# Optimization experiments

Measured on AMD Instinct MI355X. Metric: run time of the kernel, lower is better.

Reference implementation:

```python
import jax, jax.numpy as jnp
import numpy as np

B, IN, H, OUT = 1024, 512, 1024, 512   # tokens, input, hidden (MoE width), output
E, K, LAYERS = 8, 2, 10                 # experts, top-k, repeated MoE applications
EPS = 1e-10
LOSS_COEF = 0.01


def setup_inputs() -> dict:
    key = jax.random.key(0)
    ks = jax.random.split(key, 8)
    s = 0.02  # small init scale for weights
    return {
        "x": jax.random.normal(ks[0], (B, IN), jnp.float32),
        "enc_w": jax.random.normal(ks[1], (IN, H), jnp.float32) * s,
        "enc_b": jnp.zeros((H,), jnp.float32),
        "w_gate": jax.random.normal(ks[2], (H, E), jnp.float32) * s,
        "w1": jax.random.normal(ks[3], (E, H, H), jnp.float32) * s,
        "b1": jnp.zeros((E, H), jnp.float32),
        "w2": jax.random.normal(ks[4], (E, H, H), jnp.float32) * s,
        "b2": jnp.zeros((E, H), jnp.float32),
        "dec_w": jax.random.normal(ks[5], (H, OUT), jnp.float32) * s,
        "dec_b": jnp.zeros((OUT,), jnp.float32),
    }


def _cv_squared(v):
    # torch .var() is unbiased (ddof=1)
    return jnp.var(v, ddof=1) / (jnp.mean(v) ** 2 + EPS)


def _moe_layer(h, w_gate, w1, b1, w2, b2):
    # top-k gating (eval / no-noise path of noisy_top_k_gating)
    logits = h @ w_gate                                  # [B, E]
    top_vals, top_idx = jax.lax.top_k(logits, K)         # [B, K]
    gk = jax.nn.softmax(top_vals, axis=-1)               # softmax over top-k logits
    b = h.shape[0]
    gates = jnp.zeros((b, E), h.dtype).at[jnp.arange(b)[:, None], top_idx].set(gk)
    importance = gates.sum(axis=0)                       # [E]
    load = (gates > 0).sum(axis=0).astype(h.dtype)       # [E]
    aux = LOSS_COEF * (_cv_squared(importance) + _cv_squared(load))
    # experts: Linear -> ReLU -> Linear; combine weighted by gates
    # (dense-over-experts form; math identical to sparse dispatch/combine)
    hid = jax.nn.relu(jnp.einsum('bh,ehf->bef', h, w1) + b1)  # [B, E, H]
    y = jnp.einsum('bef,efo->beo', hid, w2) + b2              # [B, E, H]
    out = jnp.einsum('be,beo->bo', gates, y)                  # [B, H]
    return out, aux


def reference(x, enc_w, enc_b, w_gate, w1, b1, w2, b2, dec_w, dec_b):
    h = jax.nn.relu(x @ enc_w + enc_b)
    loss = jnp.zeros((), h.dtype)
    for _ in range(LAYERS):  # same MoE module (shared params) applied 10 times
        h, aux = _moe_layer(h, w_gate, w1, b1, w2, b2)
        loss = loss + aux
    out = jax.nn.relu(h @ dec_w + dec_b)
    return out, loss
```

## Files before the change

kernel.cpp:

```cpp
#include <hip/hip_runtime.h>
#include <math.h>

#define TPB 256
typedef unsigned short u16;
typedef unsigned int u32;
typedef __bf16 bf16x8 __attribute__((ext_vector_type(8)));
typedef float f32x4 __attribute__((ext_vector_type(4)));

namespace {
constexpr int NTOK  = 1024;
constexpr int IND   = 512;
constexpr int HD    = 1024;
constexpr int OUTD  = 512;
constexpr int NE    = 8;
constexpr int NSLOT = 2048;
}

__device__ __forceinline__ u16 f2bf(float f) {
  u32 x = __float_as_uint(f);
  x += 0x7fffu + ((x >> 16) & 1u);
  return (u16)(x >> 16);
}
__device__ __forceinline__ float bf2f(u16 u) { return __uint_as_float(((u32)u) << 16); }
__device__ __forceinline__ void split2(float v, u16& h, u16& l) {
  h = f2bf(v);
  l = f2bf(v - bf2f(h));
}

__device__ __forceinline__ void gll16(const void* g, void* l) {
  __builtin_amdgcn_global_load_lds((const __attribute__((address_space(1))) void*)g,
                                   (__attribute__((address_space(3))) void*)l, 16, 0, 0);
}


__global__ __launch_bounds__(TPB)
void transpose_split(const float* __restrict__ in, u16* __restrict__ ohi,
                     u16* __restrict__ olo, int K, int N)
{
  const int z = blockIdx.z;
  in  += (size_t)z * K * N;
  ohi += (size_t)z * K * N;
  olo += (size_t)z * K * N;
  __shared__ float tile[32][33];
  const int k0 = blockIdx.y * 32, n0 = blockIdx.x * 32;
  const int tx = threadIdx.x & 31, ty = threadIdx.x >> 5;
#pragma unroll
  for (int i = 0; i < 4; ++i) {
    int k = ty + i * 8;
    tile[k][tx] = in[(size_t)(k0 + k) * N + n0 + tx];
  }
  __syncthreads();
#pragma unroll
  for (int i = 0; i < 4; ++i) {
    int n = ty + i * 8;
    float v = tile[tx][n];
    u16 h, l; split2(v, h, l);
    int kk = k0 + tx, nn = n0 + n;
    size_t o = ((size_t)((nn >> 6) * (K >> 6) + (kk >> 6)) << 12)
             + (((nn & 63) * 8 + (((kk >> 3) & 7) ^ (nn & 7))) << 3) + (kk & 7);
    ohi[o] = h; olo[o] = l;
  }
}

__global__ __launch_bounds__(TPB)
void split_rows(const float* __restrict__ in, u16* __restrict__ oh,
                u16* __restrict__ ol, int nelem)
{
  int i = blockIdx.x * TPB + threadIdx.x;
  if (i * 4 >= nelem) return;
  float4 v = ((const float4*)in)[i];
  ushort4 H, L;
  split2(v.x, H.x, L.x); split2(v.y, H.y, L.y);
  split2(v.z, H.z, L.z); split2(v.w, H.w, L.w);
  ((ushort4*)oh)[i] = H;
  ((ushort4*)ol)[i] = L;
}

template<bool RELU, bool GROUPED, bool GATHER, bool SPLIT_OUT>
__global__ __launch_bounds__(TPB)
void gemm_split(const u16* __restrict__ Ah, const u16* __restrict__ Al,
                const int* __restrict__ gatherIdx,
                const u16* __restrict__ Bh, const u16* __restrict__ Bl,
                const float* __restrict__ bias,
                float* __restrict__ Cf, u16* __restrict__ Ch, u16* __restrict__ Cl,
                const int* __restrict__ seg_off, const int* __restrict__ seg_cnt,
                int M, int K, int N)
{
  const int e = GROUPED ? blockIdx.z : 0;
  int cnt = M, base = 0;
  if (GROUPED) { cnt = seg_cnt[e]; base = seg_off[e]; }
  const int tm = blockIdx.y, tn = blockIdx.x;
  if (tm * 64 >= cnt) return;

  __shared__ u16 smem[16384];
  constexpr int AHo = 0, ALo = 4096, BHo = 8192, BLo = 12288;

  const int t = threadIdx.x;
  const int wid = t >> 6, lane = t & 63;
  const int wr = wid >> 1, wc = wid & 1;

  const u16* aph[2]; const u16* apl[2];
#pragma unroll
  for (int i = 0; i < 2; ++i) {
    int slot = t + i * TPB;
    int row = slot >> 3, kblk = slot & 7;
    int kbs = kblk ^ (row & 7);
    int row_in = tm * 64 + row;
    int rv = row_in < cnt ? row_in : 0;
    int src;
    if (GATHER)      src = gatherIdx[base + rv];
    else             src = GROUPED ? base + rv : rv;
    size_t off = (size_t)src * K + kbs * 8;
    aph[i] = Ah + off; apl[i] = Al + off;
  }
  const u16* bsh; const u16* bsl;
  {
    size_t pb = ((size_t)((GROUPED ? e : 0) * (N >> 6) + tn) * (K >> 6)) << 12;
    bsh = Bh + pb; bsl = Bl + pb;
  }

  auto stage = [&](int ks) {
#pragma unroll
    for (int i = 0; i < 2; ++i) {
      int so = (t + i * TPB) * 8;
      gll16(aph[i] + (ks << 6), &smem[AHo + so]);
      gll16(apl[i] + (ks << 6), &smem[ALo + so]);
    }
    const size_t tb = (size_t)ks << 12;
#pragma unroll
    for (int i = 0; i < 2; ++i) {
      int so = (t + i * TPB) * 8;
      gll16(bsh + tb + so, &smem[BHo + so]);
      gll16(bsl + tb + so, &smem[BLo + so]);
    }
  };

  f32x4 acc[2][2];
#pragma unroll
  for (int i = 0; i < 2; ++i)
#pragma unroll
    for (int j = 0; j < 2; ++j) acc[i][j] = (f32x4){0.f, 0.f, 0.f, 0.f};

  auto compute = [&]() {
#pragma unroll
    for (int s = 0; s < 2; ++s) {
      const int kb = s * 4 + (lane >> 4);
      bf16x8 fah[2], fal[2];
#pragma unroll
      for (int fr = 0; fr < 2; ++fr) {
        int ar = wr * 32 + fr * 16 + (lane & 15);
        int off = ar * 64 + ((kb ^ (ar & 7)) << 3);
        fah[fr] = *(const bf16x8*)&smem[AHo + off];
        fal[fr] = *(const bf16x8*)&smem[ALo + off];
      }
      bf16x8 fbh[2], fbl[2];
#pragma unroll
      for (int fc = 0; fc < 2; ++fc) {
        int bn = wc * 32 + fc * 16 + (lane & 15);
        int off = bn * 64 + ((kb ^ (bn & 7)) << 3);
        fbh[fc] = *(const bf16x8*)&smem[BHo + off];
        fbl[fc] = *(const bf16x8*)&smem[BLo + off];
      }
      __builtin_amdgcn_s_setprio(1);
#pragma unroll
      for (int fr = 0; fr < 2; ++fr)
#pragma unroll
        for (int fc = 0; fc < 2; ++fc) {
          acc[fr][fc] = __builtin_amdgcn_mfma_f32_16x16x32_bf16(fah[fr], fbh[fc], acc[fr][fc], 0, 0, 0);
          acc[fr][fc] = __builtin_amdgcn_mfma_f32_16x16x32_bf16(fah[fr], fbl[fc], acc[fr][fc], 0, 0, 0);
          acc[fr][fc] = __builtin_amdgcn_mfma_f32_16x16x32_bf16(fal[fr], fbh[fc], acc[fr][fc], 0, 0, 0);
        }
      __builtin_amdgcn_s_setprio(0);
    }
  };

  const int NT = K >> 6;
  for (int ks = 0; ks < NT; ++ks) {
    stage(ks);
    __syncthreads();
    compute();
    __syncthreads();
  }

  const float* bp = bias + (GROUPED ? (size_t)e * N : 0);
#pragma unroll
  for (int fr = 0; fr < 2; ++fr) {
#pragma unroll
    for (int q = 0; q < 4; ++q) {
      int row_in = tm * 64 + wr * 32 + fr * 16 + ((lane >> 4) << 2) + q;
      if (row_in >= cnt) continue;
      size_t orow = (size_t)(GROUPED ? base + row_in : row_in);
#pragma unroll
      for (int fc = 0; fc < 2; ++fc) {
        int col = tn * 64 + wc * 32 + fc * 16 + (lane & 15);
        float v = acc[fr][fc][q] + bp[col];
        if (RELU) v = fmaxf(v, 0.f);
        if (SPLIT_OUT) {
          u16 h, l; split2(v, h, l);
          Ch[orow * N + col] = h;
          Cl[orow * N + col] = l;
        } else {
          Cf[orow * N + col] = v;
        }
      }
    }
  }
}

__global__ __launch_bounds__(TPB)
void gate_split(const u16* __restrict__ hh, const u16* __restrict__ hl,
                const float* __restrict__ w_gate,
                int* __restrict__ eidx, float* __restrict__ gval)
{
  const int b = blockIdx.x, t = threadIdx.x;
  ushort4 H = ((const ushort4*)(hh + (size_t)b * HD))[t];
  ushort4 L = ((const ushort4*)(hl + (size_t)b * HD))[t];
  float hv[4] = { bf2f(H.x) + bf2f(L.x), bf2f(H.y) + bf2f(L.y),
                  bf2f(H.z) + bf2f(L.z), bf2f(H.w) + bf2f(L.w) };
  float acc[NE] = {};
  const int i0 = t * 4;
#pragma unroll
  for (int j = 0; j < 4; ++j) {
    const float4* wg = (const float4*)(w_gate + (size_t)(i0 + j) * NE);
    float4 w0 = wg[0], w1 = wg[1];
    acc[0] = fmaf(hv[j], w0.x, acc[0]); acc[1] = fmaf(hv[j], w0.y, acc[1]);
    acc[2] = fmaf(hv[j], w0.z, acc[2]); acc[3] = fmaf(hv[j], w0.w, acc[3]);
    acc[4] = fmaf(hv[j], w1.x, acc[4]); acc[5] = fmaf(hv[j], w1.y, acc[5]);
    acc[6] = fmaf(hv[j], w1.z, acc[6]); acc[7] = fmaf(hv[j], w1.w, acc[7]);
  }
  __shared__ float red[TPB][NE];
#pragma unroll
  for (int e = 0; e < NE; ++e) red[t][e] = acc[e];
  __syncthreads();
  for (int s = TPB / 2; s > 0; s >>= 1) {
    if (t < s) {
#pragma unroll
      for (int e = 0; e < NE; ++e) red[t][e] += red[t + s][e];
    }
    __syncthreads();
  }
  if (t == 0) {
    float v1 = -1e30f; int e1 = 0;
#pragma unroll
    for (int e = 0; e < NE; ++e) { float v = red[0][e]; if (v > v1) { v1 = v; e1 = e; } }
    float v2 = -1e30f; int e2 = 0;
#pragma unroll
    for (int e = 0; e < NE; ++e) {
      if (e == e1) continue;
      float v = red[0][e]; if (v > v2) { v2 = v; e2 = e; }
    }
    float ev = expf(v2 - v1);
    eidx[b * 2] = e1;  eidx[b * 2 + 1] = e2;
    gval[b * 2] = 1.f / (1.f + ev);  gval[b * 2 + 1] = ev / (1.f + ev);
  }
}

__global__ __launch_bounds__(TPB)
void stats_scatter(const int* __restrict__ eidx, const float* __restrict__ gval,
                   float* __restrict__ loss, int* __restrict__ seg_off,
                   int* __restrict__ seg_cnt, int* __restrict__ slot_token,
                   int* __restrict__ slot_of)
{
  const int t = threadIdx.x;
  float imp[NE] = {};
  int   cnt[NE] = {};
  for (int s = t; s < NSLOT; s += TPB) {
    int e = eidx[s]; float g = gval[s];
#pragma unroll
    for (int q = 0; q < NE; ++q) if (q == e) { imp[q] += g; cnt[q]++; }
  }
  __shared__ float rimp[TPB][NE];
  __shared__ int   rcnt[TPB][NE];
#pragma unroll
  for (int e = 0; e < NE; ++e) { rimp[t][e] = imp[e]; rcnt[t][e] = cnt[e]; }
  __syncthreads();
  for (int s = TPB / 2; s > 0; s >>= 1) {
    if (t < s) {
#pragma unroll
      for (int e = 0; e < NE; ++e) { rimp[t][e] += rimp[t + s][e]; rcnt[t][e] += rcnt[t + s][e]; }
    }
    __syncthreads();
  }
  __shared__ int s_off[NE], s_fill[NE];
  if (t == 0) {
    float mi = 0.f, ml = 0.f;
#pragma unroll
    for (int e = 0; e < NE; ++e) { mi += rimp[0][e]; ml += (float)rcnt[0][e]; }
    mi /= NE; ml /= NE;
    float vi = 0.f, vl = 0.f;
#pragma unroll
    for (int e = 0; e < NE; ++e) {
      float di = rimp[0][e] - mi; vi += di * di;
      float dl = (float)rcnt[0][e] - ml; vl += dl * dl;
    }
    vi /= (NE - 1); vl /= (NE - 1);
    loss[0] += 0.01f * (vi / (mi * mi + 1e-10f) + vl / (ml * ml + 1e-10f));
    int off = 0;
#pragma unroll
    for (int e = 0; e < NE; ++e) {
      seg_off[e] = off; seg_cnt[e] = rcnt[0][e];
      s_off[e] = off; s_fill[e] = 0; off += rcnt[0][e];
    }
  }
  __syncthreads();
  for (int s = t; s < NSLOT; s += TPB) {
    int e = eidx[s];
    int pos = s_off[e] + atomicAdd(&s_fill[e], 1);
    slot_token[pos] = s >> 1;
    slot_of[s] = pos;
  }
}

template<bool GATE>
__global__ __launch_bounds__(TPB)
void combine_gate(const float* __restrict__ y, const float* __restrict__ gv_in,
                  const int* __restrict__ slot_of, const float* __restrict__ w_gate,
                  u16* __restrict__ hh, u16* __restrict__ hl,
                  int* __restrict__ eidx, float* __restrict__ gval)
{
  const int b = blockIdx.x, t = threadIdx.x;
  const int p0 = slot_of[b * 2], p1 = slot_of[b * 2 + 1];
  const float g0 = gv_in[b * 2], g1 = gv_in[b * 2 + 1];
  float4 a = ((const float4*)(y + (size_t)p0 * HD))[t];
  float4 c = ((const float4*)(y + (size_t)p1 * HD))[t];
  float v[4] = { g0 * a.x + g1 * c.x, g0 * a.y + g1 * c.y,
                 g0 * a.z + g1 * c.z, g0 * a.w + g1 * c.w };
  ushort4 H, L;
  split2(v[0], H.x, L.x); split2(v[1], H.y, L.y);
  split2(v[2], H.z, L.z); split2(v[3], H.w, L.w);
  ((ushort4*)(hh + (size_t)b * HD))[t] = H;
  ((ushort4*)(hl + (size_t)b * HD))[t] = L;

  if (GATE) {
    float acc[NE] = {};
    const int i0 = t * 4;
#pragma unroll
    for (int j = 0; j < 4; ++j) {
      const float4* wg = (const float4*)(w_gate + (size_t)(i0 + j) * NE);
      float4 w0 = wg[0], w1 = wg[1];
      acc[0] = fmaf(v[j], w0.x, acc[0]); acc[1] = fmaf(v[j], w0.y, acc[1]);
      acc[2] = fmaf(v[j], w0.z, acc[2]); acc[3] = fmaf(v[j], w0.w, acc[3]);
      acc[4] = fmaf(v[j], w1.x, acc[4]); acc[5] = fmaf(v[j], w1.y, acc[5]);
      acc[6] = fmaf(v[j], w1.z, acc[6]); acc[7] = fmaf(v[j], w1.w, acc[7]);
    }
    __shared__ float red[TPB][NE];
#pragma unroll
    for (int e = 0; e < NE; ++e) red[t][e] = acc[e];
    __syncthreads();
    for (int s = TPB / 2; s > 0; s >>= 1) {
      if (t < s) {
#pragma unroll
        for (int e = 0; e < NE; ++e) red[t][e] += red[t + s][e];
      }
      __syncthreads();
    }
    if (t == 0) {
      float v1 = -1e30f; int e1 = 0;
#pragma unroll
      for (int e = 0; e < NE; ++e) { float vv = red[0][e]; if (vv > v1) { v1 = vv; e1 = e; } }
      float v2 = -1e30f; int e2 = 0;
#pragma unroll
      for (int e = 0; e < NE; ++e) {
        if (e == e1) continue;
        float vv = red[0][e]; if (vv > v2) { v2 = vv; e2 = e; }
      }
      float ev = expf(v2 - v1);
      eidx[b * 2] = e1;  eidx[b * 2 + 1] = e2;
      gval[b * 2] = 1.f / (1.f + ev);  gval[b * 2 + 1] = ev / (1.f + ev);
    }
  }
}

__global__ void init_kernel(float* loss) { loss[0] = 0.f; }
__global__ void write_loss(const float* __restrict__ loss, float* __restrict__ out)
{ out[0] = loss[0]; }

template<bool RELU, bool GROUPED, bool GATHER>
__global__ __launch_bounds__(TPB)
void gemm_f32(const float* __restrict__ A, const int* __restrict__ gatherIdx,
              const float* __restrict__ B, const float* __restrict__ bias,
              float* __restrict__ C, const int* __restrict__ seg_off,
              const int* __restrict__ seg_cnt, int M, int K, int N)
{
  const int e = GROUPED ? blockIdx.z : 0;
  int cnt = M, base = 0;
  if (GROUPED) { cnt = seg_cnt[e]; base = seg_off[e]; }
  const int tm = blockIdx.y, tn = blockIdx.x;
  if (tm * 64 >= cnt) return;
  const float* Bp = B + (size_t)e * K * N;
  const float* bp = bias + (size_t)e * N;
  __shared__ float As[16][68];
  __shared__ float Bs[16][64];
  const int t = threadIdx.x;
  const int rm0 = (t >> 4) << 2, cn0 = (t & 15) << 2;
  int arow[4]; bool aval[4];
#pragma unroll
  for (int i = 0; i < 4; ++i) {
    int idx = t + i * TPB;
    int r = idx >> 4;
    int row_in = tm * 64 + r;
    bool v = row_in < cnt;
    int src;
    if (GATHER) src = v ? gatherIdx[base + row_in] : 0;
    else        src = v ? (GROUPED ? base + row_in : row_in) : 0;
    arow[i] = src; aval[i] = v;
  }
  float acc[4][4] = {};
  for (int k0 = 0; k0 < K; k0 += 16) {
#pragma unroll
    for (int i = 0; i < 4; ++i) {
      int idx = t + i * TPB;
      int r = idx >> 4, kk = idx & 15;
      As[kk][r] = aval[i] ? A[(size_t)arow[i] * K + k0 + kk] : 0.f;
    }
#pragma unroll
    for (int i = 0; i < 4; ++i) {
      int idx = t + i * TPB;
      int kk = idx >> 6, n = idx & 63;
      Bs[kk][n] = Bp[(size_t)(k0 + kk) * N + tn * 64 + n];
    }
    __syncthreads();
#pragma unroll
    for (int kk = 0; kk < 16; ++kk) {
      const float4 a4 = *(const float4*)&As[kk][rm0];
      const float4 b4 = *(const float4*)&Bs[kk][cn0];
      float av[4] = {a4.x, a4.y, a4.z, a4.w};
      float bv[4] = {b4.x, b4.y, b4.z, b4.w};
#pragma unroll
      for (int i = 0; i < 4; ++i)
#pragma unroll
        for (int j = 0; j < 4; ++j) acc[i][j] = fmaf(av[i], bv[j], acc[i][j]);
    }
    __syncthreads();
  }
#pragma unroll
  for (int i = 0; i < 4; ++i) {
    int row_in = tm * 64 + rm0 + i;
    if (row_in >= cnt) continue;
    size_t orow = (size_t)(base + row_in);
    float v0 = acc[i][0] + bp[tn * 64 + cn0 + 0];
    float v1 = acc[i][1] + bp[tn * 64 + cn0 + 1];
    float v2 = acc[i][2] + bp[tn * 64 + cn0 + 2];
    float v3 = acc[i][3] + bp[tn * 64 + cn0 + 3];
    if (RELU) { v0 = fmaxf(v0, 0.f); v1 = fmaxf(v1, 0.f); v2 = fmaxf(v2, 0.f); v3 = fmaxf(v3, 0.f); }
    *(float4*)&C[orow * N + tn * 64 + cn0] = make_float4(v0, v1, v2, v3);
  }
}

__global__ __launch_bounds__(TPB)
void gate_f32(const float* __restrict__ h, const float* __restrict__ w_gate,
              int* __restrict__ eidx, float* __restrict__ gval)
{
  const int b = blockIdx.x, t = threadIdx.x;
  float acc[NE] = {};
  const float* hb = h + (size_t)b * HD;
  for (int i = t; i < HD; i += TPB) {
    float hv = hb[i];
    const float* wg = w_gate + (size_t)i * NE;
#pragma unroll
    for (int e = 0; e < NE; ++e) acc[e] = fmaf(hv, wg[e], acc[e]);
  }
  __shared__ float red[TPB][NE];
#pragma unroll
  for (int e = 0; e < NE; ++e) red[t][e] = acc[e];
  __syncthreads();
  for (int s = TPB / 2; s > 0; s >>= 1) {
    if (t < s) {
#pragma unroll
      for (int e = 0; e < NE; ++e) red[t][e] += red[t + s][e];
    }
    __syncthreads();
  }
  if (t == 0) {
    float v1 = -1e30f; int e1 = 0;
#pragma unroll
    for (int e = 0; e < NE; ++e) { float v = red[0][e]; if (v > v1) { v1 = v; e1 = e; } }
    float v2 = -1e30f; int e2 = 0;
#pragma unroll
    for (int e = 0; e < NE; ++e) {
      if (e == e1) continue;
      float v = red[0][e]; if (v > v2) { v2 = v; e2 = e; }
    }
    float ev = expf(v2 - v1);
    eidx[b * 2] = e1;  eidx[b * 2 + 1] = e2;
    gval[b * 2] = 1.f / (1.f + ev);  gval[b * 2 + 1] = ev / (1.f + ev);
  }
}

__global__ __launch_bounds__(TPB)
void combine_f32(const float* __restrict__ y, const float* __restrict__ gval,
                 const int* __restrict__ slot_of, float* __restrict__ h)
{
  const int b = blockIdx.x, t = threadIdx.x;
  const int p0 = slot_of[b * 2], p1 = slot_of[b * 2 + 1];
  const float g0 = gval[b * 2], g1 = gval[b * 2 + 1];
  const float4* y0 = (const float4*)(y + (size_t)p0 * HD);
  const float4* y1 = (const float4*)(y + (size_t)p1 * HD);
  float4* hb = (float4*)(h + (size_t)b * HD);
  for (int i = t; i < HD / 4; i += TPB) {
    float4 a = y0[i], c = y1[i];
    hb[i] = make_float4(g0 * a.x + g1 * c.x, g0 * a.y + g1 * c.y,
                        g0 * a.z + g1 * c.z, g0 * a.w + g1 * c.w);
  }
}


extern "C" void kernel_launch(void* const* d_in, const int* in_sizes, int n_in,
                              void* d_out, int out_size, void* d_ws, size_t ws_size,
                              hipStream_t stream)
{
  const float* x      = (const float*)d_in[0];
  const float* enc_w  = (const float*)d_in[1];
  const float* enc_b  = (const float*)d_in[2];
  const float* w_gate = (const float*)d_in[3];
  const float* w1     = (const float*)d_in[4];
  const float* b1     = (const float*)d_in[5];
  const float* w2     = (const float*)d_in[6];
  const float* b2     = (const float*)d_in[7];
  const float* dec_w  = (const float*)d_in[8];
  const float* dec_b  = (const float*)d_in[9];
  float* outp = (float*)d_out;
  dim3 blk(TPB);

  const size_t NEED = 100ull << 20;
  if (ws_size >= NEED) {
    char* p = (char*)d_ws;
    auto alloc = [&](size_t bytes) { char* r = p; p += (bytes + 255) & ~(size_t)255; return r; };
    u16* w1t_h = (u16*)alloc((size_t)NE * HD * HD * 2);
    u16* w1t_l = (u16*)alloc((size_t)NE * HD * HD * 2);
    u16* w2t_h = (u16*)alloc((size_t)NE * HD * HD * 2);
    u16* w2t_l = (u16*)alloc((size_t)NE * HD * HD * 2);
    u16* ewt_h = (u16*)alloc((size_t)IND * HD * 2);
    u16* ewt_l = (u16*)alloc((size_t)IND * HD * 2);
    u16* dwt_h = (u16*)alloc((size_t)HD * OUTD * 2);
    u16* dwt_l = (u16*)alloc((size_t)HD * OUTD * 2);
    u16* x_h   = (u16*)alloc((size_t)NTOK * IND * 2);
    u16* x_l   = (u16*)alloc((size_t)NTOK * IND * 2);
    u16* h_h   = (u16*)alloc((size_t)NTOK * HD * 2);
    u16* h_l   = (u16*)alloc((size_t)NTOK * HD * 2);
    u16* hid_h = (u16*)alloc((size_t)NSLOT * HD * 2);
    u16* hid_l = (u16*)alloc((size_t)NSLOT * HD * 2);
    float* y   = (float*)alloc((size_t)NSLOT * HD * 4);
    int*   eidx       = (int*)alloc(NSLOT * 4);
    float* gval       = (float*)alloc(NSLOT * 4);
    int*   slot_of    = (int*)alloc(NSLOT * 4);
    int*   slot_token = (int*)alloc(NSLOT * 4);
    int*   seg_off    = (int*)alloc(256);
    int*   seg_cnt    = (int*)alloc(256);
    float* loss       = (float*)alloc(256);

    init_kernel<<<1, 1, 0, stream>>>(loss);
    transpose_split<<<dim3(HD / 32, HD / 32, NE), blk, 0, stream>>>(w1, w1t_h, w1t_l, HD, HD);
    transpose_split<<<dim3(HD / 32, HD / 32, NE), blk, 0, stream>>>(w2, w2t_h, w2t_l, HD, HD);
    transpose_split<<<dim3(HD / 32, IND / 32, 1), blk, 0, stream>>>(enc_w, ewt_h, ewt_l, IND, HD);
    transpose_split<<<dim3(OUTD / 32, HD / 32, 1), blk, 0, stream>>>(dec_w, dwt_h, dwt_l, HD, OUTD);
    split_rows<<<(NTOK * IND / 4 + TPB - 1) / TPB, blk, 0, stream>>>(x, x_h, x_l, NTOK * IND);

    gemm_split<true, false, false, true><<<dim3(HD / 64, NTOK / 64, 1), blk, 0, stream>>>(
        x_h, x_l, nullptr, ewt_h, ewt_l, enc_b, nullptr, h_h, h_l, nullptr, nullptr,
        NTOK, IND, HD);

    gate_split<<<NTOK, blk, 0, stream>>>(h_h, h_l, w_gate, eidx, gval);
    for (int L = 0; L < 10; ++L) {
      stats_scatter<<<1, blk, 0, stream>>>(eidx, gval, loss, seg_off, seg_cnt,
                                           slot_token, slot_of);
      gemm_split<true, true, true, true><<<dim3(HD / 64, NSLOT / 64, NE), blk, 0, stream>>>(
          h_h, h_l, slot_token, w1t_h, w1t_l, b1, nullptr, hid_h, hid_l,
          seg_off, seg_cnt, 0, HD, HD);
      gemm_split<false, true, false, false><<<dim3(HD / 64, NSLOT / 64, NE), blk, 0, stream>>>(
          hid_h, hid_l, nullptr, w2t_h, w2t_l, b2, y, nullptr, nullptr,
          seg_off, seg_cnt, 0, HD, HD);
      if (L < 9)
        combine_gate<true><<<NTOK, blk, 0, stream>>>(y, gval, slot_of, w_gate,
                                                     h_h, h_l, eidx, gval);
      else
        combine_gate<false><<<NTOK, blk, 0, stream>>>(y, gval, slot_of, w_gate,
                                                      h_h, h_l, eidx, gval);
    }

    gemm_split<true, false, false, false><<<dim3(OUTD / 64, NTOK / 64, 1), blk, 0, stream>>>(
        h_h, h_l, nullptr, dwt_h, dwt_l, dec_b, outp, nullptr, nullptr, nullptr, nullptr,
        NTOK, HD, OUTD);
    write_loss<<<1, 1, 0, stream>>>(loss, outp + NTOK * OUTD);
    return;
  }

  char* ws = (char*)d_ws;
  float* h   = (float*)(ws);
  float* hid = (float*)(ws + (4u  << 20));
  float* y   = (float*)(ws + (12u << 20));
  char* sp = ws + (20u << 20);
  int*   eidx       = (int*)sp;    sp += NSLOT * 4;
  float* gval       = (float*)sp;  sp += NSLOT * 4;
  int*   slot_of    = (int*)sp;    sp += NSLOT * 4;
  int*   slot_token = (int*)sp;    sp += NSLOT * 4;
  int*   seg_off    = (int*)sp;    sp += 64;
  int*   seg_cnt    = (int*)sp;    sp += 64;
  float* loss       = (float*)sp;  sp += 64;

  init_kernel<<<1, 1, 0, stream>>>(loss);
  gemm_f32<true, false, false><<<dim3(HD / 64, NTOK / 64, 1), blk, 0, stream>>>(
      x, nullptr, enc_w, enc_b, h, nullptr, nullptr, NTOK, IND, HD);
  for (int L = 0; L < 10; ++L) {
    gate_f32<<<NTOK, blk, 0, stream>>>(h, w_gate, eidx, gval);
    stats_scatter<<<1, blk, 0, stream>>>(eidx, gval, loss, seg_off, seg_cnt,
                                         slot_token, slot_of);
    gemm_f32<true, true, true><<<dim3(HD / 64, NTOK / 64, NE), blk, 0, stream>>>(
        h, slot_token, w1, b1, hid, seg_off, seg_cnt, 0, HD, HD);
    gemm_f32<false, true, false><<<dim3(HD / 64, NTOK / 64, NE), blk, 0, stream>>>(
        hid, nullptr, w2, b2, y, seg_off, seg_cnt, 0, HD, HD);
    combine_f32<<<NTOK, blk, 0, stream>>>(y, gval, slot_of, h);
  }
  gemm_f32<true, false, false><<<dim3(OUTD / 64, NTOK / 64, 1), blk, 0, stream>>>(
      h, nullptr, dec_w, dec_b, outp, nullptr, nullptr, NTOK, HD, OUTD);
  write_loss<<<1, 1, 0, stream>>>(loss, outp + NTOK * OUTD);
}
```

Measured before the change: 794.7 us.

## Double-buffer A tiles in LDS and load B fragments directly to registers

The split-bf16 GEMM now double-buffers the A tile in shared memory and prefetches the next k-step while computing the current one. B fragments are loaded straight from pre-swizzled global memory into registers, two register sets deep, instead of going through LDS. Manual vmcnt waits and raw barriers replace __syncthreads so loads overlap the MFMA work. This raises register pressure and depends on vmcnt counting and the pre-swizzled B layout matching the fragment offsets. It also assumes an even number of k-tiles.

```diff
diff --git a/kernel.cpp b/kernel.cpp
--- a/kernel.cpp
+++ b/kernel.cpp
@@ -93,7 +93,7 @@
   if (tm * 64 >= cnt) return;
 
   __shared__ u16 smem[16384];
-  constexpr int AHo = 0, ALo = 4096, BHo = 8192, BLo = 12288;
+  constexpr int ALo = 4096, ABUF = 8192;
 
   const int t = threadIdx.x;
   const int wid = t >> 6, lane = t & 63;
@@ -118,22 +118,32 @@
     size_t pb = ((size_t)((GROUPED ? e : 0) * (N >> 6) + tn) * (K >> 6)) << 12;
     bsh = Bh + pb; bsl = Bl + pb;
   }
-
-  auto stage = [&](int ks) {
-#pragma unroll
-    for (int i = 0; i < 2; ++i) {
-      int so = (t + i * TPB) * 8;
-      gll16(aph[i] + (ks << 6), &smem[AHo + so]);
-      gll16(apl[i] + (ks << 6), &smem[ALo + so]);
-    }
-    const size_t tb = (size_t)ks << 12;
-#pragma unroll
-    for (int i = 0; i < 2; ++i) {
-      int so = (t + i * TPB) * 8;
-      gll16(bsh + tb + so, &smem[BHo + so]);
-      gll16(bsl + tb + so, &smem[BLo + so]);
-    }
-  };
+  int bno[2], koff[2];
+#pragma unroll
+  for (int fc = 0; fc < 2; ++fc) bno[fc] = (wc * 32 + fc * 16 + (lane & 15)) * 64;
+#pragma unroll
+  for (int s = 0; s < 2; ++s) koff[s] = ((s * 4 + (lane >> 4)) ^ (lane & 7)) * 8;
+
+#define STAGE_A(BB, KS) do {                                           \
+  _Pragma("unroll")                                                    \
+  for (int i_ = 0; i_ < 2; ++i_) {                                     \
+    int so_ = (t + i_ * TPB) * 8;                                      \
+    gll16(aph[i_] + ((KS) << 6), &smem[(BB) + so_]);                   \
+    gll16(apl[i_] + ((KS) << 6), &smem[(BB) + ALo + so_]);             \
+  }                                                                    \
+} while (0)
+
+#define LOAD_B(DST, KS) do {                                           \
+  size_t tb_ = (size_t)(KS) << 12;                                     \
+  _Pragma("unroll")                                                    \
+  for (int s_ = 0; s_ < 2; ++s_)                                       \
+  _Pragma("unroll")                                                    \
+  for (int fc_ = 0; fc_ < 2; ++fc_) {                                  \
+    size_t o_ = tb_ + bno[fc_] + koff[s_];                             \
+    DST[s_ * 4 + fc_ * 2 + 0] = *(const bf16x8*)(bsh + o_);            \
+    DST[s_ * 4 + fc_ * 2 + 1] = *(const bf16x8*)(bsl + o_);            \
+  }                                                                    \
+} while (0)
 
   f32x4 acc[2][2];
 #pragma unroll
@@ -141,46 +151,56 @@
 #pragma unroll
     for (int j = 0; j < 2; ++j) acc[i][j] = (f32x4){0.f, 0.f, 0.f, 0.f};
 
-  auto compute = [&]() {
-#pragma unroll
-    for (int s = 0; s < 2; ++s) {
-      const int kb = s * 4 + (lane >> 4);
-      bf16x8 fah[2], fal[2];
-#pragma unroll
-      for (int fr = 0; fr < 2; ++fr) {
-        int ar = wr * 32 + fr * 16 + (lane & 15);
-        int off = ar * 64 + ((kb ^ (ar & 7)) << 3);
-        fah[fr] = *(const bf16x8*)&smem[AHo + off];
-        fal[fr] = *(const bf16x8*)&smem[ALo + off];
-      }
-      bf16x8 fbh[2], fbl[2];
-#pragma unroll
-      for (int fc = 0; fc < 2; ++fc) {
-        int bn = wc * 32 + fc * 16 + (lane & 15);
-        int off = bn * 64 + ((kb ^ (bn & 7)) << 3);
-        fbh[fc] = *(const bf16x8*)&smem[BHo + off];
-        fbl[fc] = *(const bf16x8*)&smem[BLo + off];
-      }
-      __builtin_amdgcn_s_setprio(1);
-#pragma unroll
-      for (int fr = 0; fr < 2; ++fr)
-#pragma unroll
-        for (int fc = 0; fc < 2; ++fc) {
-          acc[fr][fc] = __builtin_amdgcn_mfma_f32_16x16x32_bf16(fah[fr], fbh[fc], acc[fr][fc], 0, 0, 0);
-          acc[fr][fc] = __builtin_amdgcn_mfma_f32_16x16x32_bf16(fah[fr], fbl[fc], acc[fr][fc], 0, 0, 0);
-          acc[fr][fc] = __builtin_amdgcn_mfma_f32_16x16x32_bf16(fal[fr], fbh[fc], acc[fr][fc], 0, 0, 0);
-        }
-      __builtin_amdgcn_s_setprio(0);
-    }
-  };
-
+#define COMPUTE(BB, B) do {                                            \
+  _Pragma("unroll")                                                    \
+  for (int s_ = 0; s_ < 2; ++s_) {                                     \
+    const int kb_ = s_ * 4 + (lane >> 4);                              \
+    bf16x8 fah_[2], fal_[2];                                           \
+    _Pragma("unroll")                                                  \
+    for (int fr_ = 0; fr_ < 2; ++fr_) {                                \
+      int ar_ = wr * 32 + fr_ * 16 + (lane & 15);                      \
+      int off_ = (BB) + ar_ * 64 + ((kb_ ^ (ar_ & 7)) << 3);           \
+      fah_[fr_] = *(const bf16x8*)&smem[off_];                         \
+      fal_[fr_] = *(const bf16x8*)&smem[ALo + off_];                   \
+    }                                                                  \
+    __builtin_amdgcn_s_setprio(1);                                     \
+    _Pragma("unroll")                                                  \
+    for (int fr_ = 0; fr_ < 2; ++fr_)                                  \
+    _Pragma("unroll")                                                  \
+    for (int fc_ = 0; fc_ < 2; ++fc_) {                                \
+      acc[fr_][fc_] = __builtin_amdgcn_mfma_f32_16x16x32_bf16(         \
+          fah_[fr_], B[s_ * 4 + fc_ * 2 + 0], acc[fr_][fc_], 0, 0, 0); \
+      acc[fr_][fc_] = __builtin_amdgcn_mfma_f32_16x16x32_bf16(         \
+          fah_[fr_], B[s_ * 4 + fc_ * 2 + 1], acc[fr_][fc_], 0, 0, 0); \
+      acc[fr_][fc_] = __builtin_amdgcn_mfma_f32_16x16x32_bf16(         \
+          fal_[fr_], B[s_ * 4 + fc_ * 2 + 0], acc[fr_][fc_], 0, 0, 0); \
+    }                                                                  \
+    __builtin_amdgcn_s_setprio(0);                                     \
+  }                                                                    \
+} while (0)
+
+#define ITER(TT, CUR, NXT, CUROFF, NXTOFF) do {                        \
+  __builtin_amdgcn_s_barrier();            \
+  if ((TT) + 1 < NT) { STAGE_A((NXTOFF), (TT) + 1); LOAD_B(NXT, (TT) + 1); } \
+  __builtin_amdgcn_sched_barrier(0);                                   \
+  if ((TT) + 1 < NT) { asm volatile("s_waitcnt vmcnt(12)" ::: "memory"); } \
+  else               { asm volatile("s_waitcnt vmcnt(0)"  ::: "memory"); } \
+  __builtin_amdgcn_s_barrier();                     \
+  COMPUTE((CUROFF), CUR);                                              \
+} while (0)
+
+  bf16x8 bA[8], bB[8];
   const int NT = K >> 6;
-  for (int ks = 0; ks < NT; ++ks) {
-    stage(ks);
-    __syncthreads();
-    compute();
-    __syncthreads();
-  }
+  STAGE_A(0, 0);
+  LOAD_B(bA, 0);
+  for (int t2 = 0; t2 < NT; t2 += 2) {
+    ITER(t2,     bA, bB, 0,    ABUF);
+    ITER(t2 + 1, bB, bA, ABUF, 0);
+  }
+#undef ITER
+#undef COMPUTE
+#undef LOAD_B
+#undef STAGE_A
 
   const float* bp = bias + (GROUPED ? (size_t)e * N : 0);
 #pragma unroll
```

After: 916.8 us. +15.4%, slower.
